# Performance work log

Measured on AMD Instinct MI355X. Metric: run time of the kernel, lower is better.

## Reference

```python
import jax, jax.numpy as jnp
import numpy as np

HIDDEN, N_HEADS, HEAD_DIM, CACHE_LEN, BATCH = 4096, 32, 128, 512, 32


def setup_inputs() -> dict:
    key = jax.random.key(0)
    ks = jax.random.split(key, 7)
    s = 0.02
    return {
        "x": jax.random.normal(ks[0], (BATCH, 1, HIDDEN), jnp.float32),
        "k_cache": jax.random.normal(ks[1], (BATCH, N_HEADS, CACHE_LEN, HEAD_DIM), jnp.float32),
        "v_cache": jax.random.normal(ks[2], (BATCH, N_HEADS, CACHE_LEN, HEAD_DIM), jnp.float32),
        # torch nn.Linear weights: (out_features, in_features), y = x @ W.T
        "wq": jax.random.normal(ks[3], (N_HEADS * HEAD_DIM, HIDDEN), jnp.float32) * s,
        "wk": jax.random.normal(ks[4], (N_HEADS * HEAD_DIM, HIDDEN), jnp.float32) * s,
        "wv": jax.random.normal(ks[5], (N_HEADS * HEAD_DIM, HIDDEN), jnp.float32) * s,
        "wo": jax.random.normal(ks[6], (HIDDEN, N_HEADS * HEAD_DIM), jnp.float32) * s,
    }


def reference(x, k_cache, v_cache, wq, wk, wv, wo):
    bsz = x.shape[0]
    # projections: (b, 1, H*D) -> (b, n_heads, 1, head_dim)
    def proj(w):
        return (x @ w.T).reshape(bsz, 1, N_HEADS, HEAD_DIM).transpose(0, 2, 1, 3)
    q, k_new, v_new = proj(wq), proj(wk), proj(wv)
    scale = 1.0 / HEAD_DIM ** 0.5
    # cache attention: (b, h, 1, cache_len)
    cache_scores = jnp.einsum("bhqd,bhkd->bhqk", q, k_cache) * scale
    cache_probs = jax.nn.softmax(cache_scores, axis=-1)
    cache_out = jnp.einsum("bhqk,bhkd->bhqd", cache_probs, v_cache)
    # new-token attention: softmax over a single key (probs == 1), kept faithful
    new_scores = jnp.einsum("bhqd,bhkd->bhqk", q, k_new) * scale
    new_probs = jax.nn.softmax(new_scores, axis=-1)
    new_out = jnp.einsum("bhqk,bhkd->bhqd", new_probs, v_new)
    out = cache_out + new_out  # note: sum of two separately-normalized softmaxes (as in source)
    out = out.transpose(0, 2, 1, 3).reshape(bsz, 1, N_HEADS * HEAD_DIM)
    return out @ wo.T
```

## Files before the change

kernel.cpp:

```cpp
#include <hip/hip_runtime.h>
#include <hip/hip_bf16.h>

#define HIDDEN 4096
#define NHEADS 32
#define HDIM 128
#define CLEN 512
#define BATCH 32
#define KB 256

typedef float f32x4 __attribute__((ext_vector_type(4)));

__device__ __forceinline__ void proj_body(const float* __restrict__ X,
                                          const float* __restrict__ W,
                                          float* __restrict__ Y,
                                          int rowblock) {
    const int t   = threadIdx.x;
    const int l   = t & 63;
    const int wid = t >> 6;
    const int rowbase = rowblock * 8;
    const float* wp = W + (size_t)rowbase * HIDDEN + 4 * l;
    const float* xp = X + (size_t)(wid * 4) * HIDDEN + 4 * l;

    float v[32];
    #pragma unroll
    for (int j = 0; j < 32; ++j) v[j] = 0.f;

    #pragma unroll 2
    for (int kp = 0; kp < HIDDEN; kp += 256) {
        float4 wv[8], xv[4];
        #pragma unroll
        for (int r = 0; r < 8; ++r)
            wv[r] = *(const float4*)(wp + (size_t)r * HIDDEN + kp);
        #pragma unroll
        for (int b = 0; b < 4; ++b)
            xv[b] = *(const float4*)(xp + (size_t)b * HIDDEN + kp);
        #pragma unroll
        for (int r = 0; r < 8; ++r) {
            #pragma unroll
            for (int b = 0; b < 4; ++b) {
                v[r * 4 + b] += wv[r].x * xv[b].x + wv[r].y * xv[b].y +
                                wv[r].z * xv[b].z + wv[r].w * xv[b].w;
            }
        }
    }

    #pragma unroll
    for (int j = 0; j < 32; ++j) v[j] += __shfl_xor(v[j], 1);
    #pragma unroll
    for (int s = 1; s <= 5; ++s) {
        const int m = 1 << s;
        const int bit = (l >> s) & 1;
        #pragma unroll
        for (int i = 0; i < (32 >> s); ++i) {
            float t0 = __shfl_xor(v[2 * i], m);
            float t1 = __shfl_xor(v[2 * i + 1], m);
            v[i] = bit ? (v[2 * i + 1] + t1) : (v[2 * i] + t0);
        }
    }
    if (!(l & 1)) {
        const int j = l >> 1;
        const int r = j >> 2, b = j & 3;
        Y[(size_t)(wid * 4 + b) * HIDDEN + rowbase + r] = v[0];
    }
}

__global__ __launch_bounds__(512, 2) void proj_out_kernel(const float* __restrict__ X,
                                                          const float* __restrict__ W,
                                                          float* __restrict__ Y) {
    proj_body(X, W, Y, blockIdx.x);
}

__device__ __forceinline__ void proj4_body(const float* __restrict__ X,
                                           const float* __restrict__ W,
                                           float* __restrict__ Y,
                                           int rowblock) {
    const int t   = threadIdx.x;
    const int l   = t & 63;
    const int wid = t >> 6;
    const int rowbase = rowblock * 4;
    const float* wp = W + (size_t)rowbase * HIDDEN + 4 * l;
    const float* xp = X + (size_t)(wid * 8) * HIDDEN + 4 * l;

    float v[32];
    #pragma unroll
    for (int j = 0; j < 32; ++j) v[j] = 0.f;

    #pragma unroll 2
    for (int kp = 0; kp < HIDDEN; kp += 256) {
        float4 wv[4], xv[8];
        #pragma unroll
        for (int r = 0; r < 4; ++r)
            wv[r] = *(const float4*)(wp + (size_t)r * HIDDEN + kp);
        #pragma unroll
        for (int b = 0; b < 8; ++b)
            xv[b] = *(const float4*)(xp + (size_t)b * HIDDEN + kp);
        #pragma unroll
        for (int r = 0; r < 4; ++r) {
            #pragma unroll
            for (int b = 0; b < 8; ++b) {
                v[r * 8 + b] += wv[r].x * xv[b].x + wv[r].y * xv[b].y +
                                wv[r].z * xv[b].z + wv[r].w * xv[b].w;
            }
        }
    }

    #pragma unroll
    for (int j = 0; j < 32; ++j) v[j] += __shfl_xor(v[j], 1);
    #pragma unroll
    for (int s = 1; s <= 5; ++s) {
        const int m = 1 << s;
        const int bit = (l >> s) & 1;
        #pragma unroll
        for (int i = 0; i < (32 >> s); ++i) {
            float t0 = __shfl_xor(v[2 * i], m);
            float t1 = __shfl_xor(v[2 * i + 1], m);
            v[i] = bit ? (v[2 * i + 1] + t1) : (v[2 * i] + t0);
        }
    }
    if (!(l & 1)) {
        const int j = l >> 1;
        const int r = j >> 3, b = j & 7;
        Y[(size_t)(wid * 8 + b) * HIDDEN + rowbase + r] = v[0];
    }
}

__global__ __launch_bounds__(256) void proj_q_kernel(const float* __restrict__ X,
                                                     const float* __restrict__ W,
                                                     float* __restrict__ Y) {
    proj4_body(X, W, Y, blockIdx.x);
}

__device__ __forceinline__ void attn_body(const float* __restrict__ q,
                                          const float* __restrict__ kc,
                                          const float* __restrict__ vc,
                                          float* __restrict__ o_half,
                                          float* __restrict__ ms,
                                          float* __restrict__ ss,
                                          int bid) {
    __shared__ float sc[KB];
    __shared__ float red[8];
    __shared__ float part[4 * HDIM];
    const int t = threadIdx.x;
    const int w = t >> 6;
    const int l = t & 63;
    const int bh = bid >> 1;
    const int half = bid & 1;
    const int b = bh >> 5, h = bh & 31;
    const float* K = kc + (size_t)bh * CLEN * HDIM + (size_t)(half * KB) * HDIM;
    const float* V = vc + (size_t)bh * CLEN * HDIM + (size_t)(half * KB) * HDIM;
    const float scale = 0.088388347648318447f;
    const int d0 = 4 * (l & 31);
    const int kh = l >> 5;
    const int start = ((bid * 37) & 127) * 2;
    float4 q4 = *(const float4*)(q + (size_t)b * HIDDEN + h * HDIM + d0);

    const int kw = w * 64;
    #pragma unroll 8
    for (int r = 0; r < 32; ++r) {
        const int k = (((kw + 2 * r) + start) & (KB - 1)) + kh;
        f32x4 kv = __builtin_nontemporal_load((const f32x4*)(K + (size_t)k * HDIM + d0));
        float p = q4.x * kv.x + q4.y * kv.y + q4.z * kv.z + q4.w * kv.w;
        #pragma unroll
        for (int m = 16; m; m >>= 1) p += __shfl_xor(p, m);
        if ((l & 31) == 0) sc[k] = p * scale;
    }
    __syncthreads();

    float s = sc[t];
    float mx = s;
    #pragma unroll
    for (int m = 32; m; m >>= 1) mx = fmaxf(mx, __shfl_xor(mx, m));
    if (l == 0) red[w] = mx;
    __syncthreads();
    mx = fmaxf(fmaxf(red[0], red[1]), fmaxf(red[2], red[3]));
    float e = __expf(s - mx);
    sc[t] = e;
    float es = e;
    #pragma unroll
    for (int m = 32; m; m >>= 1) es += __shfl_xor(es, m);
    if (l == 0) red[4 + w] = es;
    __syncthreads();
    if (t == 0) {
        ms[bid] = mx;
        ss[bid] = red[4] + red[5] + red[6] + red[7];
    }

    float4 acc = make_float4(0.f, 0.f, 0.f, 0.f);
    #pragma unroll 8
    for (int kk = 0; kk < 64; kk += 2) {
        const int k = (((kw + kk) + start) & (KB - 1)) + kh;
        f32x4 v4 = __builtin_nontemporal_load((const f32x4*)(V + (size_t)k * HDIM + d0));
        float p = sc[k];
        acc.x += p * v4.x; acc.y += p * v4.y;
        acc.z += p * v4.z; acc.w += p * v4.w;
    }
    acc.x += __shfl_xor(acc.x, 32);
    acc.y += __shfl_xor(acc.y, 32);
    acc.z += __shfl_xor(acc.z, 32);
    acc.w += __shfl_xor(acc.w, 32);
    if (l < 32) *(float4*)(&part[w * HDIM + d0]) = acc;
    __syncthreads();
    if (t < HDIM) {
        float r = part[t] + part[HDIM + t] + part[2 * HDIM + t] + part[3 * HDIM + t];
        o_half[(size_t)bid * HDIM + t] = r;
    }
}

__global__ __launch_bounds__(256) void attn_projv_kernel(
        const float* __restrict__ q, const float* __restrict__ kc,
        const float* __restrict__ vc, const float* __restrict__ x,
        const float* __restrict__ wv_m, float* __restrict__ vnew,
        float* __restrict__ o_half, float* __restrict__ ms,
        float* __restrict__ ss) {
    const int bid = blockIdx.x;
    const int sel = bid % 3;
    if (sel == 2) {
        proj4_body(x, wv_m, vnew, bid / 3);
        return;
    }
    attn_body(q, kc, vc, o_half, ms, ss, (bid / 3) * 2 + sel);
}

__global__ __launch_bounds__(256) void combine_kernel(
        const float* __restrict__ o_half,
        const float* __restrict__ ms,
        const float* __restrict__ ss,
        const float* __restrict__ vnew,
        float* __restrict__ attn_out) {
    const int t = threadIdx.x;
    const int bh = blockIdx.x * 2 + (t >> 7);
    const int d = t & 127;
    const float m0 = ms[2 * bh], m1 = ms[2 * bh + 1];
    const float s0 = ss[2 * bh], s1 = ss[2 * bh + 1];
    const float M = fmaxf(m0, m1);
    const float w0 = __expf(m0 - M), w1 = __expf(m1 - M);
    const float inv = 1.0f / (s0 * w0 + s1 * w1);
    const float o0 = o_half[(size_t)(2 * bh) * HDIM + d];
    const float o1 = o_half[(size_t)(2 * bh + 1) * HDIM + d];
    const int b = bh >> 5, h = bh & 31;
    const size_t idx = (size_t)b * HIDDEN + h * HDIM + d;
    attn_out[idx] = (o0 * w0 + o1 * w1) * inv + vnew[idx];
}

extern "C" void kernel_launch(void* const* d_in, const int* in_sizes, int n_in,
                              void* d_out, int out_size, void* d_ws, size_t ws_size,
                              hipStream_t stream) {
    (void)in_sizes; (void)n_in; (void)out_size; (void)ws_size;
    const float* x  = (const float*)d_in[0];
    const float* kc = (const float*)d_in[1];
    const float* vc = (const float*)d_in[2];
    const float* wq = (const float*)d_in[3];
    const float* wv = (const float*)d_in[5];
    const float* wo = (const float*)d_in[6];
    float* out = (float*)d_out;

    float* q      = (float*)d_ws;
    float* vnew   = q + BATCH * HIDDEN;
    float* attn   = vnew + BATCH * HIDDEN;
    float* o_half = attn + BATCH * HIDDEN;
    float* ms     = o_half + 2 * BATCH * NHEADS * HDIM;
    float* ss     = ms + 2 * BATCH * NHEADS;

    proj_q_kernel<<<HIDDEN / 4, 256, 0, stream>>>(x, wq, q);
    attn_projv_kernel<<<3072, 256, 0, stream>>>(q, kc, vc, x, wv, vnew,
                                                o_half, ms, ss);
    combine_kernel<<<BATCH * NHEADS / 2, 256, 0, stream>>>(o_half, ms, ss, vnew, attn);
    proj_out_kernel<<<HIDDEN / 8, 512, 0, stream>>>(attn, wo, out);
}
```

Before: 185.9 us.

## Use per-wave online softmax in attention, combining eight partials per head

Replaces the block-level two-pass softmax, which stored scores in shared memory and used several barriers, with a per-wave online softmax. Each wave loads K and V rows together and keeps a running max, sum and accumulator. Each wave writes its own partial (8 per head), and the combine kernel merges them with log-sum-exp weights. This removes the shared memory and __syncthreads, letting K and V loads overlap, at the cost of two exps per key and more partial data written and read. It also adds a launch-bounds occupancy hint.

Result: no change. 185.3 us (-0.3%).

```diff
diff --git a/kernel.cpp b/kernel.cpp
--- a/kernel.cpp
+++ b/kernel.cpp
@@ -133,84 +133,65 @@
 __device__ __forceinline__ void attn_body(const float* __restrict__ q,
                                           const float* __restrict__ kc,
                                           const float* __restrict__ vc,
-                                          float* __restrict__ o_half,
+                                          float* __restrict__ o_part,
                                           float* __restrict__ ms,
                                           float* __restrict__ ss,
                                           int bid) {
-    __shared__ float sc[KB];
-    __shared__ float red[8];
-    __shared__ float part[4 * HDIM];
     const int t = threadIdx.x;
     const int w = t >> 6;
     const int l = t & 63;
     const int bh = bid >> 1;
     const int half = bid & 1;
     const int b = bh >> 5, h = bh & 31;
-    const float* K = kc + (size_t)bh * CLEN * HDIM + (size_t)(half * KB) * HDIM;
-    const float* V = vc + (size_t)bh * CLEN * HDIM + (size_t)(half * KB) * HDIM;
+    const float* K = kc + (size_t)bh * CLEN * HDIM + (size_t)(half * KB + w * 64) * HDIM;
+    const float* V = vc + (size_t)bh * CLEN * HDIM + (size_t)(half * KB + w * 64) * HDIM;
     const float scale = 0.088388347648318447f;
     const int d0 = 4 * (l & 31);
     const int kh = l >> 5;
-    const int start = ((bid * 37) & 127) * 2;
-    float4 q4 = *(const float4*)(q + (size_t)b * HIDDEN + h * HDIM + d0);
-
-    const int kw = w * 64;
-    #pragma unroll 8
+    const int rot = (bid & 31) * 2;
+    f32x4 q4 = *(const f32x4*)(q + (size_t)b * HIDDEN + h * HDIM + d0);
+
+    float mloc = -INFINITY, sloc = 0.f;
+    f32x4 acc = {0.f, 0.f, 0.f, 0.f};
+
+    #pragma unroll 4
     for (int r = 0; r < 32; ++r) {
-        const int k = (((kw + 2 * r) + start) & (KB - 1)) + kh;
+        const int k = ((2 * r + rot) & 63) + kh;
         f32x4 kv = __builtin_nontemporal_load((const f32x4*)(K + (size_t)k * HDIM + d0));
         float p = q4.x * kv.x + q4.y * kv.y + q4.z * kv.z + q4.w * kv.w;
         #pragma unroll
         for (int m = 16; m; m >>= 1) p += __shfl_xor(p, m);
-        if ((l & 31) == 0) sc[k] = p * scale;
-    }
-    __syncthreads();
-
-    float s = sc[t];
-    float mx = s;
-    #pragma unroll
-    for (int m = 32; m; m >>= 1) mx = fmaxf(mx, __shfl_xor(mx, m));
-    if (l == 0) red[w] = mx;
-    __syncthreads();
-    mx = fmaxf(fmaxf(red[0], red[1]), fmaxf(red[2], red[3]));
-    float e = __expf(s - mx);
-    sc[t] = e;
-    float es = e;
-    #pragma unroll
-    for (int m = 32; m; m >>= 1) es += __shfl_xor(es, m);
-    if (l == 0) red[4 + w] = es;
-    __syncthreads();
-    if (t == 0) {
-        ms[bid] = mx;
-        ss[bid] = red[4] + red[5] + red[6] + red[7];
-    }
-
-    float4 acc = make_float4(0.f, 0.f, 0.f, 0.f);
-    #pragma unroll 8
-    for (int kk = 0; kk < 64; kk += 2) {
-        const int k = (((kw + kk) + start) & (KB - 1)) + kh;
-        f32x4 v4 = __builtin_nontemporal_load((const f32x4*)(V + (size_t)k * HDIM + d0));
-        float p = sc[k];
-        acc.x += p * v4.x; acc.y += p * v4.y;
-        acc.z += p * v4.z; acc.w += p * v4.w;
-    }
+        p *= scale;
+        f32x4 vv = __builtin_nontemporal_load((const f32x4*)(V + (size_t)k * HDIM + d0));
+        const float mn = fmaxf(mloc, p);
+        const float c = __expf(mloc - mn);
+        const float e = __expf(p - mn);
+        sloc = sloc * c + e;
+        acc = acc * c + vv * e;
+        mloc = mn;
+    }
+
+    const float mo = __shfl_xor(mloc, 32);
+    const float M = fmaxf(mloc, mo);
+    const float wsc = __expf(mloc - M);
+    float sw = sloc * wsc;
+    sw += __shfl_xor(sw, 32);
+    acc *= wsc;
     acc.x += __shfl_xor(acc.x, 32);
     acc.y += __shfl_xor(acc.y, 32);
     acc.z += __shfl_xor(acc.z, 32);
     acc.w += __shfl_xor(acc.w, 32);
-    if (l < 32) *(float4*)(&part[w * HDIM + d0]) = acc;
-    __syncthreads();
-    if (t < HDIM) {
-        float r = part[t] + part[HDIM + t] + part[2 * HDIM + t] + part[3 * HDIM + t];
-        o_half[(size_t)bid * HDIM + t] = r;
-    }
-}
-
-__global__ __launch_bounds__(256) void attn_projv_kernel(
+
+    const int pid = bh * 8 + half * 4 + w;
+    if (l < 32) *(f32x4*)(o_part + (size_t)pid * HDIM + d0) = acc;
+    if (l == 0) { ms[pid] = M; ss[pid] = sw; }
+}
+
+__global__ __launch_bounds__(256, 4) void attn_projv_kernel(
         const float* __restrict__ q, const float* __restrict__ kc,
         const float* __restrict__ vc, const float* __restrict__ x,
         const float* __restrict__ wv_m, float* __restrict__ vnew,
-        float* __restrict__ o_half, float* __restrict__ ms,
+        float* __restrict__ o_part, float* __restrict__ ms,
         float* __restrict__ ss) {
     const int bid = blockIdx.x;
     const int sel = bid % 3;
@@ -218,11 +199,11 @@
         proj4_body(x, wv_m, vnew, bid / 3);
         return;
     }
-    attn_body(q, kc, vc, o_half, ms, ss, (bid / 3) * 2 + sel);
+    attn_body(q, kc, vc, o_part, ms, ss, (bid / 3) * 2 + sel);
 }
 
 __global__ __launch_bounds__(256) void combine_kernel(
-        const float* __restrict__ o_half,
+        const float* __restrict__ o_part,
         const float* __restrict__ ms,
         const float* __restrict__ ss,
         const float* __restrict__ vnew,
@@ -230,16 +211,22 @@
     const int t = threadIdx.x;
     const int bh = blockIdx.x * 2 + (t >> 7);
     const int d = t & 127;
-    const float m0 = ms[2 * bh], m1 = ms[2 * bh + 1];
-    const float s0 = ss[2 * bh], s1 = ss[2 * bh + 1];
-    const float M = fmaxf(m0, m1);
-    const float w0 = __expf(m0 - M), w1 = __expf(m1 - M);
-    const float inv = 1.0f / (s0 * w0 + s1 * w1);
-    const float o0 = o_half[(size_t)(2 * bh) * HDIM + d];
-    const float o1 = o_half[(size_t)(2 * bh + 1) * HDIM + d];
+    float m[8];
+    #pragma unroll
+    for (int j = 0; j < 8; ++j) m[j] = ms[bh * 8 + j];
+    float M = m[0];
+    #pragma unroll
+    for (int j = 1; j < 8; ++j) M = fmaxf(M, m[j]);
+    float ssum = 0.f, o = 0.f;
+    #pragma unroll
+    for (int j = 0; j < 8; ++j) {
+        const float wj = __expf(m[j] - M);
+        ssum += ss[bh * 8 + j] * wj;
+        o += o_part[(size_t)(bh * 8 + j) * HDIM + d] * wj;
+    }
     const int b = bh >> 5, h = bh & 31;
     const size_t idx = (size_t)b * HIDDEN + h * HDIM + d;
-    attn_out[idx] = (o0 * w0 + o1 * w1) * inv + vnew[idx];
+    attn_out[idx] = o / ssum + vnew[idx];
 }
 
 extern "C" void kernel_launch(void* const* d_in, const int* in_sizes, int n_in,
@@ -257,13 +244,13 @@
     float* q      = (float*)d_ws;
     float* vnew   = q + BATCH * HIDDEN;
     float* attn   = vnew + BATCH * HIDDEN;
-    float* o_half = attn + BATCH * HIDDEN;
-    float* ms     = o_half + 2 * BATCH * NHEADS * HDIM;
-    float* ss     = ms + 2 * BATCH * NHEADS;
+    float* o_part = attn + BATCH * HIDDEN;
+    float* ms     = o_part + 8 * BATCH * NHEADS * HDIM;
+    float* ss     = ms + 8 * BATCH * NHEADS;
 
     proj_q_kernel<<<HIDDEN / 4, 256, 0, stream>>>(x, wq, q);
     attn_projv_kernel<<<3072, 256, 0, stream>>>(q, kc, vc, x, wv, vnew,
-                                                o_half, ms, ss);
-    combine_kernel<<<BATCH * NHEADS / 2, 256, 0, stream>>>(o_half, ms, ss, vnew, attn);
+                                                o_part, ms, ss);
+    combine_kernel<<<BATCH * NHEADS / 2, 256, 0, stream>>>(o_part, ms, ss, vnew, attn);
     proj_out_kernel<<<HIDDEN / 8, 512, 0, stream>>>(attn, wo, out);
 }
```
